# Kernel optimization log

Measured on AMD Instinct MI355X. Metric: run time of the kernel, lower is better.

Reference implementation:

```python
import jax, jax.numpy as jnp
import numpy as np

B, D, T, K = 8, 512, 2048, 8192


def setup_inputs() -> dict:
    key = jax.random.key(0)
    k1, k2 = jax.random.split(key)
    latents = jax.random.normal(k1, (B, D, T), dtype=jnp.float32)
    # nn.Embedding weight initialized uniform(-1/K, 1/K)
    embedding = jax.random.uniform(k2, (K, D), dtype=jnp.float32,
                                   minval=-1.0 / K, maxval=1.0 / K)
    return {"latents": latents, "embedding": embedding}


def reference(latents, embedding):
    # latents: [B, D, T] -> [B, T, D]
    x = jnp.transpose(latents, (0, 2, 1))
    # argmin over squared distance == argmin over cdist(p=2), so output matches torch.
    x_sq = jnp.sum(x * x, axis=-1, keepdims=True)            # [B, T, 1]
    e_sq = jnp.sum(embedding * embedding, axis=-1)           # [K]
    cross = jnp.einsum("btd,kd->btk", x, embedding)          # [B, T, K]
    dist2 = x_sq - 2.0 * cross + e_sq                        # [B, T, K]
    encoding_inds = jnp.argmin(dist2, axis=-1)               # [B, T] int
    quantized = embedding[encoding_inds]                     # [B, T, D]
    return jnp.transpose(quantized, (0, 2, 1))               # [B, D, T]
```

## Files before the change

kernel.cpp:

```cpp
#include <hip/hip_runtime.h>
#include <hip/hip_bf16.h>
#include <cstdint>

constexpr int Dv = 512;
constexpr int Tv = 2048;
constexpr int Kv = 8192;
constexpr int BT = 16384;

constexpr int BQ = 128;
constexpr int BK = 128;
constexpr int BD = 64;
constexpr int KSPL = 4;
constexpr int KPS = Kv / KSPL;

__global__ void vq_xsq(const float* __restrict__ lat, float* __restrict__ xsq) {
    int q = blockIdx.x * 256 + threadIdx.x;
    int b = q >> 11, t = q & 2047;
    const float* p = lat + (size_t)b * Dv * Tv + t;
    float a = 0.f;
    #pragma unroll 8
    for (int d = 0; d < Dv; ++d) {
        float v = p[(size_t)d * Tv];
        a = fmaf(v, v, a);
    }
    xsq[q] = a;
}

__global__ void vq_esq(const float* __restrict__ emb, float* __restrict__ esq) {
    int gid = blockIdx.x * 256 + threadIdx.x;
    int k = gid >> 6;
    int l = threadIdx.x & 63;
    const float* p = emb + (size_t)k * Dv + l;
    float a = 0.f;
    #pragma unroll
    for (int i = 0; i < 8; ++i) {
        float v = p[i * 64];
        a = fmaf(v, v, a);
    }
    #pragma unroll
    for (int off = 32; off; off >>= 1) a += __shfl_down(a, off, 64);
    if (l == 0) esq[k] = a;
}

__global__ __launch_bounds__(256, 2) void vq_main(
        const float* __restrict__ lat, const float* __restrict__ emb,
        const float* __restrict__ xsq, const float* __restrict__ esq,
        float* __restrict__ pval, int* __restrict__ pidx) {
    __shared__ float Xs[BD][BQ];
    __shared__ float Es[BD][BK + 4];

    const int tid = threadIdx.x;
    const int bid = blockIdx.x;
    const int qb = bid & 127;
    const int ks = bid >> 7;
    const int q0 = qb * BQ;
    const int b  = q0 >> 11;
    const int t0 = q0 & 2047;
    const int k0base = ks * KPS;

    const int tx = (tid & 7) | (((tid >> 6) & 1) << 3);
    const int ty = ((tid >> 3) & 7) | (((tid >> 7) & 1) << 3);

    const int sq   = tid & 31;
    const int srow = tid >> 5;
    const int ef   = tid & 15;
    const int ekk  = tid >> 4;

    float best[8];
    int   bidx[8];
    float xs[8];
    #pragma unroll
    for (int i = 0; i < 8; ++i) {
        best[i] = 3.4e38f;
        bidx[i] = 0x7fffffff;
        xs[i] = xsq[q0 + ty * 8 + i];
    }

    const float* latb = lat + (size_t)b * Dv * Tv + t0;

    for (int kc = 0; kc < KPS / BK; ++kc) {
        const int k0 = k0base + kc * BK;
        float c[8][8];
        #pragma unroll
        for (int i = 0; i < 8; ++i)
            #pragma unroll
            for (int j = 0; j < 8; ++j) c[i][j] = 0.f;

        for (int dc = 0; dc < Dv / BD; ++dc) {
            const int d0 = dc * BD;
            __syncthreads();
            #pragma unroll
            for (int i = 0; i < 8; ++i) {
                int dd = srow + i * 8;
                float4 v = *(const float4*)(latb + (size_t)(d0 + dd) * Tv + sq * 4);
                *(float4*)&Xs[dd][sq * 4] = v;
            }
            #pragma unroll
            for (int i = 0; i < 8; ++i) {
                int kk = ekk + i * 16;
                float4 v = *(const float4*)(emb + (size_t)(k0 + kk) * Dv + d0 + ef * 4);
                Es[ef * 4 + 0][kk] = v.x;
                Es[ef * 4 + 1][kk] = v.y;
                Es[ef * 4 + 2][kk] = v.z;
                Es[ef * 4 + 3][kk] = v.w;
            }
            __syncthreads();

            #pragma unroll 4
            for (int dd = 0; dd < BD; ++dd) {
                float4 xa = *(const float4*)&Xs[dd][ty * 8];
                float4 xb = *(const float4*)&Xs[dd][ty * 8 + 4];
                float4 ea = *(const float4*)&Es[dd][tx * 8];
                float4 eb = *(const float4*)&Es[dd][tx * 8 + 4];
                float x8[8] = {xa.x, xa.y, xa.z, xa.w, xb.x, xb.y, xb.z, xb.w};
                float e8[8] = {ea.x, ea.y, ea.z, ea.w, eb.x, eb.y, eb.z, eb.w};
                #pragma unroll
                for (int i = 0; i < 8; ++i)
                    #pragma unroll
                    for (int j = 0; j < 8; ++j)
                        c[i][j] = fmaf(x8[i], e8[j], c[i][j]);
            }
        }

        float es8[8];
        #pragma unroll
        for (int j = 0; j < 8; ++j) es8[j] = esq[k0 + tx * 8 + j];
        #pragma unroll
        for (int i = 0; i < 8; ++i)
            #pragma unroll
            for (int j = 0; j < 8; ++j) {
                float dist = fmaf(-2.0f, c[i][j], xs[i]) + es8[j];
                int kk = k0 + tx * 8 + j;
                if (dist < best[i]) { best[i] = dist; bidx[i] = kk; }
            }
    }

    __syncthreads();
    float* redv = &Xs[0][0];
    int*   redi = (int*)&Es[0][0];
    #pragma unroll
    for (int i = 0; i < 8; ++i) {
        redv[(ty * 16 + tx) * 8 + i] = best[i];
        redi[(ty * 16 + tx) * 8 + i] = bidx[i];
    }
    __syncthreads();
    if (tid < 128) {
        int yy = tid >> 3, ii = tid & 7;
        float bv = 3.4e38f;
        int bi = 0x7fffffff;
        #pragma unroll
        for (int t = 0; t < 16; ++t) {
            float v = redv[(yy * 16 + t) * 8 + ii];
            int  ix = redi[(yy * 16 + t) * 8 + ii];
            if (v < bv || (v == bv && ix < bi)) { bv = v; bi = ix; }
        }
        int q = q0 + yy * 8 + ii;
        pval[(size_t)q * KSPL + ks] = bv;
        pidx[(size_t)q * KSPL + ks] = bi;
    }
}

__global__ void vq_merge(const float* __restrict__ pval, const int* __restrict__ pidx,
                         int* __restrict__ idxf) {
    int q = blockIdx.x * 256 + threadIdx.x;
    float bv = 3.4e38f;
    int bi = 0x7fffffff;
    #pragma unroll
    for (int s = 0; s < KSPL; ++s) {
        float v = pval[(size_t)q * KSPL + s];
        int  ix = pidx[(size_t)q * KSPL + s];
        if (v < bv || (v == bv && ix < bi)) { bv = v; bi = ix; }
    }
    idxf[q] = bi;
}

__global__ void vq_gather(const float* __restrict__ emb, const int* __restrict__ idxf,
                          float* __restrict__ out) {
    int blk = blockIdx.x;
    int tid = threadIdx.x;
    int tl = tid & 63, dg = tid >> 6;
    int q = blk * 64 + tl;
    int b = q >> 11, t = q & 2047;
    int idx = idxf[q];
    const float* er = emb + (size_t)idx * Dv + dg * 128;
    float* ob = out + ((size_t)b * Dv + dg * 128) * Tv + t;
    #pragma unroll 8
    for (int i = 0; i < 128; ++i) ob[(size_t)i * Tv] = er[i];
}

extern "C" void kernel_launch(void* const* d_in, const int* in_sizes, int n_in,
                              void* d_out, int out_size, void* d_ws, size_t ws_size,
                              hipStream_t stream) {
    (void)in_sizes; (void)n_in; (void)out_size; (void)ws_size;
    const float* lat = (const float*)d_in[0];
    const float* emb = (const float*)d_in[1];
    float* out = (float*)d_out;

    char* ws = (char*)d_ws;
    float* xsq  = (float*)(ws);
    float* esq  = (float*)(ws + (64 << 10));
    float* pval = (float*)(ws + (96 << 10));
    int*   pidx = (int*)  (ws + (96 << 10) + (256 << 10));
    int*   idxf = (int*)  (ws + (96 << 10) + (512 << 10));

    vq_xsq  <<<BT / 256, 256, 0, stream>>>(lat, xsq);
    vq_esq  <<<Kv / 4,   256, 0, stream>>>(emb, esq);
    vq_main <<<(BT / BQ) * KSPL, 256, 0, stream>>>(lat, emb, xsq, esq, pval, pidx);
    vq_merge<<<BT / 256, 256, 0, stream>>>(pval, pidx, idxf);
    vq_gather<<<BT / 64, 256, 0, stream>>>(emb, idxf, out);
}
```

Baseline: 1.893 ms.

## Raise occupancy, swizzle codebook tile, and merge K-splits with 64-bit atomicMin

Halves the D-chunk depth and doubles the K-split count so vq_main launches more blocks with a smaller shared-memory footprint. Launch bounds now request 4 blocks per CU. The padded codebook tile is replaced by an XOR-swizzled layout to avoid LDS bank conflicts without padding. The separate merge kernel is removed: each block packs (distance bits, index) into a 64-bit key and does atomicMin, after a small init kernel, which relies on distances being non-negative for correct ordering. The tighter register budget may cause spilling of the 8x8 accumulator tile.

```diff
diff --git a/kernel.cpp b/kernel.cpp
--- a/kernel.cpp
+++ b/kernel.cpp
@@ -9,8 +9,8 @@
 
 constexpr int BQ = 128;
 constexpr int BK = 128;
-constexpr int BD = 64;
-constexpr int KSPL = 4;
+constexpr int BD = 32;
+constexpr int KSPL = 8;
 constexpr int KPS = Kv / KSPL;
 
 __global__ void vq_xsq(const float* __restrict__ lat, float* __restrict__ xsq) {
@@ -42,12 +42,17 @@
     if (l == 0) esq[k] = a;
 }
 
-__global__ __launch_bounds__(256, 2) void vq_main(
+__global__ void vq_init(unsigned long long* __restrict__ keys) {
+    int q = blockIdx.x * 256 + threadIdx.x;
+    keys[q] = 0xFFFFFFFFFFFFFFFFull;
+}
+
+__global__ __launch_bounds__(256, 4) void vq_main(
         const float* __restrict__ lat, const float* __restrict__ emb,
         const float* __restrict__ xsq, const float* __restrict__ esq,
-        float* __restrict__ pval, int* __restrict__ pidx) {
+        unsigned long long* __restrict__ keys) {
     __shared__ float Xs[BD][BQ];
-    __shared__ float Es[BD][BK + 4];
+    __shared__ float Es[BD][BK];
 
     const int tid = threadIdx.x;
     const int bid = blockIdx.x;
@@ -63,8 +68,9 @@
 
     const int sq   = tid & 31;
     const int srow = tid >> 5;
-    const int ef   = tid & 15;
-    const int ekk  = tid >> 4;
+    const int dq   = tid & 7;
+    const int ekk  = tid >> 3;
+    const int fsw  = dq << 2;
 
     float best[8];
     int   bidx[8];
@@ -77,6 +83,7 @@
     }
 
     const float* latb = lat + (size_t)b * Dv * Tv + t0;
+    float* const esw = &Es[0][0];
 
     for (int kc = 0; kc < KPS / BK; ++kc) {
         const int k0 = k0base + kc * BK;
@@ -90,35 +97,42 @@
             const int d0 = dc * BD;
             __syncthreads();
             #pragma unroll
-            for (int i = 0; i < 8; ++i) {
+            for (int i = 0; i < 4; ++i) {
                 int dd = srow + i * 8;
                 float4 v = *(const float4*)(latb + (size_t)(d0 + dd) * Tv + sq * 4);
                 *(float4*)&Xs[dd][sq * 4] = v;
             }
             #pragma unroll
-            for (int i = 0; i < 8; ++i) {
-                int kk = ekk + i * 16;
-                float4 v = *(const float4*)(emb + (size_t)(k0 + kk) * Dv + d0 + ef * 4);
-                Es[ef * 4 + 0][kk] = v.x;
-                Es[ef * 4 + 1][kk] = v.y;
-                Es[ef * 4 + 2][kk] = v.z;
-                Es[ef * 4 + 3][kk] = v.w;
+            for (int i = 0; i < 4; ++i) {
+                int kk = ekk + i * 32;
+                float4 v = *(const float4*)(emb + (size_t)(k0 + kk) * Dv + d0 + dq * 4);
+                int ksw = kk ^ fsw;
+                esw[(dq * 4 + 0) * BK + ksw] = v.x;
+                esw[(dq * 4 + 1) * BK + ksw] = v.y;
+                esw[(dq * 4 + 2) * BK + ksw] = v.z;
+                esw[(dq * 4 + 3) * BK + ksw] = v.w;
             }
             __syncthreads();
 
             #pragma unroll 4
             for (int dd = 0; dd < BD; ++dd) {
-                float4 xa = *(const float4*)&Xs[dd][ty * 8];
-                float4 xb = *(const float4*)&Xs[dd][ty * 8 + 4];
-                float4 ea = *(const float4*)&Es[dd][tx * 8];
-                float4 eb = *(const float4*)&Es[dd][tx * 8 + 4];
-                float x8[8] = {xa.x, xa.y, xa.z, xa.w, xb.x, xb.y, xb.z, xb.w};
-                float e8[8] = {ea.x, ea.y, ea.z, ea.w, eb.x, eb.y, eb.z, eb.w};
-                #pragma unroll
-                for (int i = 0; i < 8; ++i)
-                    #pragma unroll
-                    for (int j = 0; j < 8; ++j)
-                        c[i][j] = fmaf(x8[i], e8[j], c[i][j]);
+                const int g = (dd >> 2) << 2;
+                const float4 xa = *(const float4*)&Xs[dd][ty * 8];
+                const float4 xb = *(const float4*)&Xs[dd][ty * 8 + 4];
+                const float4 ea = *(const float4*)&esw[dd * BK + ((tx * 8) ^ g)];
+                const float4 eb = *(const float4*)&esw[dd * BK + ((tx * 8 + 4) ^ g)];
+                #define VQ_ROW(i, XV)                       \
+                    c[i][0] = fmaf(XV, ea.x, c[i][0]);      \
+                    c[i][1] = fmaf(XV, ea.y, c[i][1]);      \
+                    c[i][2] = fmaf(XV, ea.z, c[i][2]);      \
+                    c[i][3] = fmaf(XV, ea.w, c[i][3]);      \
+                    c[i][4] = fmaf(XV, eb.x, c[i][4]);      \
+                    c[i][5] = fmaf(XV, eb.y, c[i][5]);      \
+                    c[i][6] = fmaf(XV, eb.z, c[i][6]);      \
+                    c[i][7] = fmaf(XV, eb.w, c[i][7]);
+                VQ_ROW(0, xa.x) VQ_ROW(1, xa.y) VQ_ROW(2, xa.z) VQ_ROW(3, xa.w)
+                VQ_ROW(4, xb.x) VQ_ROW(5, xb.y) VQ_ROW(6, xb.z) VQ_ROW(7, xb.w)
+                #undef VQ_ROW
             }
         }
 
@@ -155,33 +169,21 @@
             if (v < bv || (v == bv && ix < bi)) { bv = v; bi = ix; }
         }
         int q = q0 + yy * 8 + ii;
-        pval[(size_t)q * KSPL + ks] = bv;
-        pidx[(size_t)q * KSPL + ks] = bi;
-    }
-}
-
-__global__ void vq_merge(const float* __restrict__ pval, const int* __restrict__ pidx,
-                         int* __restrict__ idxf) {
-    int q = blockIdx.x * 256 + threadIdx.x;
-    float bv = 3.4e38f;
-    int bi = 0x7fffffff;
-    #pragma unroll
-    for (int s = 0; s < KSPL; ++s) {
-        float v = pval[(size_t)q * KSPL + s];
-        int  ix = pidx[(size_t)q * KSPL + s];
-        if (v < bv || (v == bv && ix < bi)) { bv = v; bi = ix; }
-    }
-    idxf[q] = bi;
-}
-
-__global__ void vq_gather(const float* __restrict__ emb, const int* __restrict__ idxf,
+        unsigned long long key =
+            ((unsigned long long)__float_as_uint(bv) << 32) | (unsigned int)bi;
+        atomicMin(&keys[q], key);
+    }
+}
+
+__global__ void vq_gather(const float* __restrict__ emb,
+                          const unsigned long long* __restrict__ keys,
                           float* __restrict__ out) {
     int blk = blockIdx.x;
     int tid = threadIdx.x;
     int tl = tid & 63, dg = tid >> 6;
     int q = blk * 64 + tl;
     int b = q >> 11, t = q & 2047;
-    int idx = idxf[q];
+    int idx = (int)(keys[q] & 0xFFFFFFFFull);
     const float* er = emb + (size_t)idx * Dv + dg * 128;
     float* ob = out + ((size_t)b * Dv + dg * 128) * Tv + t;
     #pragma unroll 8
@@ -197,15 +199,14 @@
     float* out = (float*)d_out;
 
     char* ws = (char*)d_ws;
-    float* xsq  = (float*)(ws);
-    float* esq  = (float*)(ws + (64 << 10));
-    float* pval = (float*)(ws + (96 << 10));
-    int*   pidx = (int*)  (ws + (96 << 10) + (256 << 10));
-    int*   idxf = (int*)  (ws + (96 << 10) + (512 << 10));
-
+    float* xsq = (float*)(ws);
+    float* esq = (float*)(ws + (64 << 10));
+    unsigned long long* keys =
+        (unsigned long long*)(ws + (96 << 10));
+
+    vq_init <<<BT / 256, 256, 0, stream>>>(keys);
     vq_xsq  <<<BT / 256, 256, 0, stream>>>(lat, xsq);
     vq_esq  <<<Kv / 4,   256, 0, stream>>>(emb, esq);
-    vq_main <<<(BT / BQ) * KSPL, 256, 0, stream>>>(lat, emb, xsq, esq, pval, pidx);
-    vq_merge<<<BT / 256, 256, 0, stream>>>(pval, pidx, idxf);
-    vq_gather<<<BT / 64, 256, 0, stream>>>(emb, idxf, out);
-}
+    vq_main <<<(BT / BQ) * KSPL, 256, 0, stream>>>(lat, emb, xsq, esq, keys);
+    vq_gather<<<BT / 64, 256, 0, stream>>>(emb, keys, out);
+}
```

Measured after the change: 2.061 ms. 1.09x slower.
